# Kernel tuning notes

Hardware: AMD Instinct MI355X
Metric: run time of the kernel (lower is better)

The kernel has to match this reference:

```python
import jax, jax.numpy as jnp
import numpy as np

NUM_HEADS = 16
D_K = 8          # = n_wires in _QLayer
EMBED_DIM = NUM_HEADS * D_K
BATCH, SEQ = 8, 1024


def quantum_heads(x, theta):
    """Exact analytic simulation of the per-head 8-qubit circuit.

    Circuit per head vector v (len 8): RX(v_i) encoding on wire i, then
    trainable RX(theta_i) on wire i (RX angles add on |0>), then CNOT chain
    (0->1),(1->2),...,(6->7),(7->0), then <PauliZ> on every wire.

    Before the CNOTs each qubit is cos(a/2)|0> - i sin(a/2)|1> with
    a_i = v_i + theta_i, so bit_i ~ Bernoulli(sin^2(a_i/2)) independently and
    E[(-1)^{bit_i}] = cos(a_i). The CNOT chain is a permutation of basis
    states acting linearly over GF(2): output bit w is the XOR of input bits
    dep(w), where dep(0) = {1..7} and dep(w) = {0..w} for w>=1. Hence
    <Z_w> = prod_{j in dep(w)} cos(a_j).
    """
    b, s, e = x.shape
    a = x.reshape(b, s, NUM_HEADS, D_K) + theta      # [b,s,h,8]
    c = jnp.cos(a)
    cp = jnp.cumprod(c, axis=-1)                     # prefix products c0..cw
    z0 = jnp.prod(c[..., 1:], axis=-1, keepdims=True)  # wire 0: cos(a1)...cos(a7)
    z = jnp.concatenate([z0, cp[..., 1:]], axis=-1)  # [b,s,h,8]
    return z.reshape(b, s, e)


def setup_inputs() -> dict:
    key = jax.random.key(0)
    k1, k2, k3 = jax.random.split(key, 3)
    x = jax.random.normal(k1, (BATCH, SEQ, EMBED_DIM), dtype=jnp.float32)
    theta = jax.random.normal(k2, (D_K,), dtype=jnp.float32)
    w_combine = jax.random.normal(k3, (EMBED_DIM, EMBED_DIM), dtype=jnp.float32) * 0.05
    return {"x": x, "theta": theta, "w_combine": w_combine}


def reference(x, theta, w_combine):
    b, s, e = x.shape
    # The module calls the SAME _QLayer on the same x three times, so q=k=v.
    meas = quantum_heads(x, theta)                                   # [b,s,e]
    qkv = meas.reshape(b, s, NUM_HEADS, D_K).transpose(0, 2, 1, 3)   # [b,h,s,d]
    scores = jnp.einsum('bhqd,bhkd->bhqk', qkv, qkv) / np.float32(np.sqrt(D_K))
    attn = jax.nn.softmax(scores, axis=-1)
    out = jnp.einsum('bhqk,bhkd->bhqd', attn, qkv)
    out = out.transpose(0, 2, 1, 3).reshape(b, s, e)
    return out @ w_combine.T  # bias-free combine_heads Linear
```

## Files before the change

### kernel.cpp

```cpp
#include <hip/hip_runtime.h>
#include <hip/hip_bf16.h>

#define NUM_HEADS 16
#define D_K 8
#define EMBED 128
#define BATCH 8
#define SEQ 1024
#define ROWS (BATCH*SEQ)
#define BH (BATCH*NUM_HEADS)
#define INV_SQRT_DK 0.35355339059327373f

__global__ __launch_bounds__(256) void k_qlayer(const float* __restrict__ x,
                                                const float* __restrict__ theta,
                                                float* __restrict__ qkv) {
    int idx = blockIdx.x * 256 + threadIdx.x;
    int b = idx >> 14;
    int h = (idx >> 10) & 15;
    int s = idx & 1023;

    const float* xp = x + ((size_t)((b << 10) + s)) * 128 + h * 8;
    float4 v0 = *(const float4*)xp;
    float4 v1 = *(const float4*)(xp + 4);

    float c0 = cosf(v0.x + theta[0]);
    float c1 = cosf(v0.y + theta[1]);
    float c2 = cosf(v0.z + theta[2]);
    float c3 = cosf(v0.w + theta[3]);
    float c4 = cosf(v1.x + theta[4]);
    float c5 = cosf(v1.y + theta[5]);
    float c6 = cosf(v1.z + theta[6]);
    float c7 = cosf(v1.w + theta[7]);

    float z1 = c0 * c1;
    float z2 = z1 * c2;
    float z3 = z2 * c3;
    float z4 = z3 * c4;
    float z5 = z4 * c5;
    float z6 = z5 * c6;
    float z7 = z6 * c7;
    float z0 = c1 * c2;
    z0 *= c3; z0 *= c4; z0 *= c5; z0 *= c6; z0 *= c7;

    float* op = qkv + (size_t)idx * 8;
    *(float4*)op       = make_float4(z0, z1, z2, z3);
    *(float4*)(op + 4) = make_float4(z4, z5, z6, z7);
}

__global__ __launch_bounds__(256) void k_wt(const float* __restrict__ w,
                                            float* __restrict__ wt) {
    int idx = blockIdx.x * 256 + threadIdx.x;
    int e = idx >> 7;
    int f = idx & 127;
    wt[f * 128 + e] = w[idx];
}

__global__ __launch_bounds__(256) void k_attn(const float* __restrict__ qkv,
                                              float* __restrict__ attn_out) {
    __shared__ float kv[SEQ * 8];
    int bx = blockIdx.x;
    int bh = bx >> 2;
    int qc = bx & 3;
    int t = threadIdx.x;

    const float4* src = (const float4*)(qkv + (size_t)bh * SEQ * 8);
    float4* dst = (float4*)kv;
#pragma unroll
    for (int i = 0; i < 8; ++i)
        dst[t + 256 * i] = src[t + 256 * i];
    __syncthreads();

    int row = qc * 256 + t;
    float q[8];
#pragma unroll
    for (int i = 0; i < 8; ++i)
        q[i] = kv[row * 8 + i] * INV_SQRT_DK;

    float o0 = 0.f, o1 = 0.f, o2 = 0.f, o3 = 0.f;
    float o4 = 0.f, o5 = 0.f, o6 = 0.f, o7 = 0.f;
    float sum = 0.f;

#pragma unroll 4
    for (int j = 0; j < SEQ; ++j) {
        float4 k0 = *(const float4*)&kv[j * 8];
        float4 k1 = *(const float4*)&kv[j * 8 + 4];
        float s = q[0] * k0.x + q[1] * k0.y + q[2] * k0.z + q[3] * k0.w
                + q[4] * k1.x + q[5] * k1.y + q[6] * k1.z + q[7] * k1.w;
        float p = __expf(s);
        sum += p;
        o0 += p * k0.x; o1 += p * k0.y; o2 += p * k0.z; o3 += p * k0.w;
        o4 += p * k1.x; o5 += p * k1.y; o6 += p * k1.z; o7 += p * k1.w;
    }

    float inv = 1.0f / sum;
    int b = bh >> 4, h = bh & 15;
    float* op = attn_out + ((size_t)(b * SEQ + row)) * 128 + h * 8;
    *(float4*)op       = make_float4(o0 * inv, o1 * inv, o2 * inv, o3 * inv);
    *(float4*)(op + 4) = make_float4(o4 * inv, o5 * inv, o6 * inv, o7 * inv);
}

__global__ __launch_bounds__(256) void k_combine(const float* __restrict__ a,
                                                 const float* __restrict__ wt,
                                                 float* __restrict__ out) {
    int t = threadIdx.x;
    int e = t & 127;
    int half = t >> 7;
    size_t r0 = (size_t)blockIdx.x * 8 + half * 4;
    const float* arow = a + r0 * 128;

    float acc0 = 0.f, acc1 = 0.f, acc2 = 0.f, acc3 = 0.f;
#pragma unroll 4
    for (int f = 0; f < 128; ++f) {
        float wv = wt[f * 128 + e];
        acc0 += arow[f]       * wv;
        acc1 += arow[128 + f] * wv;
        acc2 += arow[256 + f] * wv;
        acc3 += arow[384 + f] * wv;
    }
    out[(r0 + 0) * 128 + e] = acc0;
    out[(r0 + 1) * 128 + e] = acc1;
    out[(r0 + 2) * 128 + e] = acc2;
    out[(r0 + 3) * 128 + e] = acc3;
}

extern "C" void kernel_launch(void* const* d_in, const int* in_sizes, int n_in,
                              void* d_out, int out_size, void* d_ws, size_t ws_size,
                              hipStream_t stream) {
    const float* x     = (const float*)d_in[0];
    const float* theta = (const float*)d_in[1];
    const float* w     = (const float*)d_in[2];
    float* out = (float*)d_out;

    float* qkv  = (float*)d_ws;
    float* attn = qkv + (size_t)BH * SEQ * 8;
    float* wt   = attn + (size_t)ROWS * EMBED;

    k_qlayer<<<(BH * SEQ) / 256, 256, 0, stream>>>(x, theta, qkv);
    k_wt<<<(EMBED * EMBED) / 256, 256, 0, stream>>>(w, wt);
    k_attn<<<BH * 4, 256, 0, stream>>>(qkv, attn);
    k_combine<<<ROWS / 8, 256, 0, stream>>>(attn, wt, out);
}
```

Before: 166.6 us.

## Fuse quantum layer into attention, process two queries per thread, use exp2

Measured after the change: 165.3 us. No clear change (-0.8%).

```diff
diff --git a/kernel.cpp b/kernel.cpp
--- a/kernel.cpp
+++ b/kernel.cpp
@@ -2,49 +2,17 @@
 #include <hip/hip_bf16.h>
 
 #define NUM_HEADS 16
-#define D_K 8
 #define EMBED 128
 #define BATCH 8
 #define SEQ 1024
 #define ROWS (BATCH*SEQ)
-#define BH (BATCH*NUM_HEADS)
-#define INV_SQRT_DK 0.35355339059327373f
+#define QSCALE 0.5101256830f
 
-__global__ __launch_bounds__(256) void k_qlayer(const float* __restrict__ x,
-                                                const float* __restrict__ theta,
-                                                float* __restrict__ qkv) {
-    int idx = blockIdx.x * 256 + threadIdx.x;
-    int b = idx >> 14;
-    int h = (idx >> 10) & 15;
-    int s = idx & 1023;
-
-    const float* xp = x + ((size_t)((b << 10) + s)) * 128 + h * 8;
-    float4 v0 = *(const float4*)xp;
-    float4 v1 = *(const float4*)(xp + 4);
-
-    float c0 = cosf(v0.x + theta[0]);
-    float c1 = cosf(v0.y + theta[1]);
-    float c2 = cosf(v0.z + theta[2]);
-    float c3 = cosf(v0.w + theta[3]);
-    float c4 = cosf(v1.x + theta[4]);
-    float c5 = cosf(v1.y + theta[5]);
-    float c6 = cosf(v1.z + theta[6]);
-    float c7 = cosf(v1.w + theta[7]);
-
-    float z1 = c0 * c1;
-    float z2 = z1 * c2;
-    float z3 = z2 * c3;
-    float z4 = z3 * c4;
-    float z5 = z4 * c5;
-    float z6 = z5 * c6;
-    float z7 = z6 * c7;
-    float z0 = c1 * c2;
-    z0 *= c3; z0 *= c4; z0 *= c5; z0 *= c6; z0 *= c7;
-
-    float* op = qkv + (size_t)idx * 8;
-    *(float4*)op       = make_float4(z0, z1, z2, z3);
-    *(float4*)(op + 4) = make_float4(z4, z5, z6, z7);
-}
+#if __has_builtin(__builtin_amdgcn_exp2f)
+#define EXP2(x) __builtin_amdgcn_exp2f(x)
+#else
+#define EXP2(x) exp2f(x)
+#endif
 
 __global__ __launch_bounds__(256) void k_wt(const float* __restrict__ w,
                                             float* __restrict__ wt) {
@@ -54,48 +22,88 @@
     wt[f * 128 + e] = w[idx];
 }
 
-__global__ __launch_bounds__(256) void k_attn(const float* __restrict__ qkv,
-                                              float* __restrict__ attn_out) {
-    __shared__ float kv[SEQ * 8];
-    int bx = blockIdx.x;
-    int bh = bx >> 2;
-    int qc = bx & 3;
-    int t = threadIdx.x;
+__global__ __launch_bounds__(256) void k_attn(const float* __restrict__ x,
+                                              const float* __restrict__ theta,
+                                              float* __restrict__ attn) {
+    __shared__ __align__(16) float z[SEQ * 8];
+    const int bid = blockIdx.x;
+    const int bh = bid >> 1, qh = bid & 1;
+    const int b = bh >> 4, h = bh & 15;
+    const int t = threadIdx.x;
 
-    const float4* src = (const float4*)(qkv + (size_t)bh * SEQ * 8);
-    float4* dst = (float4*)kv;
+    float th[8];
 #pragma unroll
-    for (int i = 0; i < 8; ++i)
-        dst[t + 256 * i] = src[t + 256 * i];
+    for (int i = 0; i < 8; ++i) th[i] = theta[i];
+
+    float q[2][8];
+#pragma unroll
+    for (int j = 0; j < 4; ++j) {
+        int r = t + 256 * j;
+        const float* xp = x + ((size_t)((b << 10) + r)) * 128 + h * 8;
+        float4 a0 = *(const float4*)xp;
+        float4 a1 = *(const float4*)(xp + 4);
+        float c0 = cosf(a0.x + th[0]);
+        float c1 = cosf(a0.y + th[1]);
+        float c2 = cosf(a0.z + th[2]);
+        float c3 = cosf(a0.w + th[3]);
+        float c4 = cosf(a1.x + th[4]);
+        float c5 = cosf(a1.y + th[5]);
+        float c6 = cosf(a1.z + th[6]);
+        float c7 = cosf(a1.w + th[7]);
+        float z1 = c0 * c1;
+        float z2 = z1 * c2;
+        float z3 = z2 * c3;
+        float z4 = z3 * c4;
+        float z5 = z4 * c5;
+        float z6 = z5 * c6;
+        float z7 = z6 * c7;
+        float z0 = c1 * c2;
+        z0 *= c3; z0 *= c4; z0 *= c5; z0 *= c6; z0 *= c7;
+        *(float4*)&z[r * 8]     = make_float4(z0, z1, z2, z3);
+        *(float4*)&z[r * 8 + 4] = make_float4(z4, z5, z6, z7);
+        if ((j >> 1) == qh) {
+            int jj = j & 1;
+            q[jj][0] = z0 * QSCALE; q[jj][1] = z1 * QSCALE;
+            q[jj][2] = z2 * QSCALE; q[jj][3] = z3 * QSCALE;
+            q[jj][4] = z4 * QSCALE; q[jj][5] = z5 * QSCALE;
+            q[jj][6] = z6 * QSCALE; q[jj][7] = z7 * QSCALE;
+        }
+    }
     __syncthreads();
 
-    int row = qc * 256 + t;
-    float q[8];
+    float o[2][8];
 #pragma unroll
-    for (int i = 0; i < 8; ++i)
-        q[i] = kv[row * 8 + i] * INV_SQRT_DK;
-
-    float o0 = 0.f, o1 = 0.f, o2 = 0.f, o3 = 0.f;
-    float o4 = 0.f, o5 = 0.f, o6 = 0.f, o7 = 0.f;
-    float sum = 0.f;
+    for (int jj = 0; jj < 2; ++jj)
+#pragma unroll
+        for (int i = 0; i < 8; ++i) o[jj][i] = 0.f;
+    float sm0 = 0.f, sm1 = 0.f;
 
 #pragma unroll 4
-    for (int j = 0; j < SEQ; ++j) {
-        float4 k0 = *(const float4*)&kv[j * 8];
-        float4 k1 = *(const float4*)&kv[j * 8 + 4];
-        float s = q[0] * k0.x + q[1] * k0.y + q[2] * k0.z + q[3] * k0.w
-                + q[4] * k1.x + q[5] * k1.y + q[6] * k1.z + q[7] * k1.w;
-        float p = __expf(s);
-        sum += p;
-        o0 += p * k0.x; o1 += p * k0.y; o2 += p * k0.z; o3 += p * k0.w;
-        o4 += p * k1.x; o5 += p * k1.y; o6 += p * k1.z; o7 += p * k1.w;
+    for (int kk = 0; kk < SEQ; ++kk) {
+        float4 k0 = *(const float4*)&z[kk * 8];
+        float4 k1 = *(const float4*)&z[kk * 8 + 4];
+        float s0 = q[0][0]*k0.x + q[0][1]*k0.y + q[0][2]*k0.z + q[0][3]*k0.w
+                 + q[0][4]*k1.x + q[0][5]*k1.y + q[0][6]*k1.z + q[0][7]*k1.w;
+        float s1 = q[1][0]*k0.x + q[1][1]*k0.y + q[1][2]*k0.z + q[1][3]*k0.w
+                 + q[1][4]*k1.x + q[1][5]*k1.y + q[1][6]*k1.z + q[1][7]*k1.w;
+        float p0 = EXP2(s0);
+        float p1 = EXP2(s1);
+        sm0 += p0; sm1 += p1;
+        o[0][0] += p0*k0.x; o[0][1] += p0*k0.y; o[0][2] += p0*k0.z; o[0][3] += p0*k0.w;
+        o[0][4] += p0*k1.x; o[0][5] += p0*k1.y; o[0][6] += p0*k1.z; o[0][7] += p0*k1.w;
+        o[1][0] += p1*k0.x; o[1][1] += p1*k0.y; o[1][2] += p1*k0.z; o[1][3] += p1*k0.w;
+        o[1][4] += p1*k1.x; o[1][5] += p1*k1.y; o[1][6] += p1*k1.z; o[1][7] += p1*k1.w;
     }
 
-    float inv = 1.0f / sum;
-    int b = bh >> 4, h = bh & 15;
-    float* op = attn_out + ((size_t)(b * SEQ + row)) * 128 + h * 8;
-    *(float4*)op       = make_float4(o0 * inv, o1 * inv, o2 * inv, o3 * inv);
-    *(float4*)(op + 4) = make_float4(o4 * inv, o5 * inv, o6 * inv, o7 * inv);
+    float inv0 = 1.0f / sm0;
+    float inv1 = 1.0f / sm1;
+    int r0 = qh * 512 + t;
+    float* op = attn + ((size_t)((b << 10) + r0)) * 128 + h * 8;
+    *(float4*)op       = make_float4(o[0][0]*inv0, o[0][1]*inv0, o[0][2]*inv0, o[0][3]*inv0);
+    *(float4*)(op + 4) = make_float4(o[0][4]*inv0, o[0][5]*inv0, o[0][6]*inv0, o[0][7]*inv0);
+    op += (size_t)256 * 128;
+    *(float4*)op       = make_float4(o[1][0]*inv1, o[1][1]*inv1, o[1][2]*inv1, o[1][3]*inv1);
+    *(float4*)(op + 4) = make_float4(o[1][4]*inv1, o[1][5]*inv1, o[1][6]*inv1, o[1][7]*inv1);
 }
 
 __global__ __launch_bounds__(256) void k_combine(const float* __restrict__ a,
@@ -130,12 +138,10 @@
     const float* w     = (const float*)d_in[2];
     float* out = (float*)d_out;
 
-    float* qkv  = (float*)d_ws;
-    float* attn = qkv + (size_t)BH * SEQ * 8;
-    float* wt   = attn + (size_t)ROWS * EMBED;
+    float* attn = (float*)d_ws;
+    float* wt   = (float*)((char*)d_ws + (size_t)ROWS * EMBED * 4);
 
-    k_qlayer<<<(BH * SEQ) / 256, 256, 0, stream>>>(x, theta, qkv);
-    k_wt<<<(EMBED * EMBED) / 256, 256, 0, stream>>>(w, wt);
-    k_attn<<<BH * 4, 256, 0, stream>>>(qkv, attn);
+    k_wt<<<64, 256, 0, stream>>>(w, wt);
+    k_attn<<<256, 256, 0, stream>>>(x, theta, attn);
     k_combine<<<ROWS / 8, 256, 0, stream>>>(attn, wt, out);
 }
```
